# Kernel tuning notes

Hardware: AMD Instinct MI355X
Metric: run time of the kernel (lower is better)

Reference implementation:

```python
import jax, jax.numpy as jnp
import numpy as np


def setup_inputs() -> dict:
    key = jax.random.key(0)
    k1, k2 = jax.random.split(key)
    B, S, H, D = 4, 4096, 2048, 3
    hidden_states = jax.random.normal(k1, (B, S, H), dtype=jnp.float32)
    theta = jax.random.normal(k2, (D, H), dtype=jnp.float32)  # routing_params stacked [D,H]
    return {"hidden_states": hidden_states, "theta": theta}


def reference(hidden_states, theta):
    B, S, H = hidden_states.shape
    D = theta.shape[0]
    k = max(1, int(S * (1.0 / D)))  # tokens kept per depth step

    # Per-depth gemv scoring + sigmoid, all depths at once: [B,S,D]
    scores = jax.nn.sigmoid(jnp.einsum('bsh,dh->bsd', hidden_states, theta))

    depth = jnp.zeros((B, S), dtype=jnp.int32)
    active = jnp.ones((B, S), dtype=bool)
    bidx = jnp.arange(B)[:, None]  # [B,1] for batched scatter
    neg_inf = jnp.float32(-jnp.inf)

    for r in range(D):  # D is small and fixed (3)
        masked = jnp.where(active, scores[:, :, r], neg_inf)
        _, idx = jax.lax.top_k(masked, k)  # [B,k]
        depth = depth.at[bidx, idx].set(r + 1)
        step_mask = jnp.zeros((B, S), dtype=bool).at[bidx, idx].set(True)
        active = active & step_mask

    depth = jnp.where(depth == 0, 1, depth)

    # Balancing loss: note the original applies sigmoid twice (scores_list is
    # post-sigmoid, then compute_balancing_loss sigmoids again). batchmean over D.
    probs = jax.nn.sigmoid(scores).mean(axis=(0, 1))  # [D]
    target = jnp.float32(1.0 / D)
    balancing_loss = jnp.sum(target * (jnp.log(target) - jnp.log(probs))) / D

    # masks list: [ones, final_active, final_active] stacked as [D,B,S]
    masks = jnp.stack([jnp.ones((B, S), dtype=bool) if r == 0 else active
                       for r in range(D)])
    return depth, balancing_loss, masks
```

## Files before the change

### kernel.cpp

```cpp
#include <hip/hip_runtime.h>
#include <math.h>

#define BB 4
#define SS 4096
#define HH 2048
#define DD 3
#define KK 1365
#define ONEBITS 0x3f800000u
#define NW 8
#define NBLK (BB * SS / NW)

__global__ __launch_bounds__(512, 8) void score_kernel(
    const float* __restrict__ hs, const float* __restrict__ theta,
    float* __restrict__ scores0, double* __restrict__ partials,
    float* __restrict__ m0)
{
    __shared__ __align__(16) float th[DD * HH];
    __shared__ double wpart[NW][DD];

    const int tid = threadIdx.x;

    {
        const float4* src = reinterpret_cast<const float4*>(theta);
        float4* dst = reinterpret_cast<float4*>(th);
#pragma unroll
        for (int i = 0; i < 3; ++i) dst[tid + 512 * i] = src[tid + 512 * i];
    }

    const long gid = (long)blockIdx.x * 512 + tid;
    if (gid < (long)BB * SS) m0[gid] = 1.0f;

    __syncthreads();

    const int wave = tid >> 6;
    const int lane = tid & 63;
    const long token = (long)blockIdx.x * NW + wave;

    const float4* row = reinterpret_cast<const float4*>(hs + token * HH);
    const float4* t0p = reinterpret_cast<const float4*>(th);
    const float4* t1p = reinterpret_cast<const float4*>(th + HH);
    const float4* t2p = reinterpret_cast<const float4*>(th + 2 * HH);

    double a0 = 0.0, a1 = 0.0, a2 = 0.0;
#pragma unroll
    for (int j = 0; j < HH / 256; ++j) {
        const int v = j * 64 + lane;
        const float4 h  = row[v];
        const float4 x0 = t0p[v];
        const float4 x1 = t1p[v];
        const float4 x2 = t2p[v];
        a0 += (double)h.x * x0.x + (double)h.y * x0.y + (double)h.z * x0.z + (double)h.w * x0.w;
        a1 += (double)h.x * x1.x + (double)h.y * x1.y + (double)h.z * x1.z + (double)h.w * x1.w;
        a2 += (double)h.x * x2.x + (double)h.y * x2.y + (double)h.z * x2.z + (double)h.w * x2.w;
    }
#pragma unroll
    for (int off = 32; off; off >>= 1) {
        a0 += __shfl_down(a0, off);
        a1 += __shfl_down(a1, off);
        a2 += __shfl_down(a2, off);
    }

    if (lane == 0) {
        const float x0 = (float)a0, x1 = (float)a1, x2 = (float)a2;
        const float s0 = 1.0f / (1.0f + expf(-x0));
        const float s1 = 1.0f / (1.0f + expf(-x1));
        const float s2 = 1.0f / (1.0f + expf(-x2));
        scores0[token] = s0;
        wpart[wave][0] = (double)(1.0f / (1.0f + expf(-s0)));
        wpart[wave][1] = (double)(1.0f / (1.0f + expf(-s1)));
        wpart[wave][2] = (double)(1.0f / (1.0f + expf(-s2)));
    }
    __syncthreads();
    if (tid < DD) {
        const int d = tid;
        double s = 0.0;
#pragma unroll
        for (int w = 0; w < NW; ++w) s += wpart[w][d];
        partials[(long)blockIdx.x * DD + d] = s;
    }
}

__global__ __launch_bounds__(1024) void select_kernel(
    const float* __restrict__ scores0, const double* __restrict__ partials,
    float* __restrict__ out)
{
    const int tid  = threadIdx.x;
    const int lane = tid & 63;
    const int wid  = tid >> 6;
    const int blk  = blockIdx.x;

    if (blk == 12) {
        double a0 = 0.0, a1 = 0.0, a2 = 0.0;
        for (int i = tid; i < NBLK; i += 1024) {
            a0 += partials[(long)i * DD + 0];
            a1 += partials[(long)i * DD + 1];
            a2 += partials[(long)i * DD + 2];
        }
#pragma unroll
        for (int off = 32; off; off >>= 1) {
            a0 += __shfl_down(a0, off);
            a1 += __shfl_down(a1, off);
            a2 += __shfl_down(a2, off);
        }
        __shared__ double shl[DD][16];
        if (lane == 0) { shl[0][wid] = a0; shl[1][wid] = a1; shl[2][wid] = a2; }
        __syncthreads();
        if (tid == 0) {
            double p0 = 0, p1 = 0, p2 = 0;
            for (int w = 0; w < 16; ++w) { p0 += shl[0][w]; p1 += shl[1][w]; p2 += shl[2][w]; }
            const double n = (double)BB * SS;
            p0 /= n; p1 /= n; p2 /= n;
            const double t = 1.0 / 3.0;
            out[(long)BB * SS] = (float)((t * (log(t) - log(p0)) +
                                          t * (log(t) - log(p1)) +
                                          t * (log(t) - log(p2))) / 3.0);
        }
        return;
    }

    const int b = blk / 3, plane = blk % 3;
    const float* rowp = scores0 + (long)b * SS;

    __shared__ unsigned wsum[16];
    __shared__ __align__(16) unsigned su[SS];
    __shared__ unsigned whist[16 * 256];
    __shared__ unsigned wtot[4];
    __shared__ unsigned sbin, skk;

    uint4 uu = reinterpret_cast<const uint4*>(rowp)[tid];

    unsigned vstar = ONEBITS;
    unsigned e0 = (uu.x == vstar), e1 = (uu.y == vstar),
             e2 = (uu.z == vstar), e3 = (uu.w == vstar);
    unsigned cnt = e0 + e1 + e2 + e3;

    unsigned inc = cnt;
#pragma unroll
    for (int off = 1; off < 64; off <<= 1) {
        unsigned t = __shfl_up(inc, off);
        if (lane >= off) inc += t;
    }
    if (lane == 63) wsum[wid] = inc;
    __syncthreads();
    if (wid == 0) {
        unsigned wv = (lane < 16) ? wsum[lane] : 0;
#pragma unroll
        for (int off = 1; off < 16; off <<= 1) {
            unsigned t = __shfl_up(wv, off);
            if (lane >= off) wv += t;
        }
        if (lane < 16) wsum[lane] = wv;
    }
    __syncthreads();
    unsigned p     = inc - cnt + (wid > 0 ? wsum[wid - 1] : 0);
    unsigned total = wsum[15];
    unsigned rem   = KK;

    if (total < KK) {
        for (int i = tid; i < SS; i += 1024) su[i] = __float_as_uint(rowp[i]);
        unsigned prefix = 0, maskbits = 0, kk = KK;
        for (int pass = 0; pass < 4; ++pass) {
            const int shift = 24 - 8 * pass;
            for (int i = tid; i < 16 * 256; i += 1024) whist[i] = 0;
            __syncthreads();
            for (int i = tid; i < SS; i += 1024) {
                unsigned u = su[i];
                if ((u & maskbits) == prefix)
                    atomicAdd(&whist[(wid << 8) + ((u >> shift) & 255u)], 1u);
            }
            __syncthreads();
            unsigned val = 0, s = 0;
            if (tid < 256) {
                for (int w = 0; w < 16; ++w) val += whist[(w << 8) + tid];
                s = val;
#pragma unroll
                for (int off = 1; off < 64; off <<= 1) {
                    unsigned t = __shfl_down(s, off);
                    if (lane + off < 64) s += t;
                }
                if (lane == 0) wtot[wid] = s;
            }
            __syncthreads();
            if (tid < 256) {
                unsigned cge = s;
                for (int w = wid + 1; w < 4; ++w) cge += wtot[w];
                unsigned cgt = cge - val;
                if (cgt < kk && cge >= kk) { sbin = (unsigned)tid; skk = kk - cgt; }
            }
            __syncthreads();
            prefix   |= (sbin << shift);
            maskbits |= (255u << shift);
            kk = skk;
        }
        vstar = prefix;
        rem   = kk;
        e0 = (uu.x == vstar); e1 = (uu.y == vstar);
        e2 = (uu.z == vstar); e3 = (uu.w == vstar);
        cnt = e0 + e1 + e2 + e3;
        inc = cnt;
#pragma unroll
        for (int off = 1; off < 64; off <<= 1) {
            unsigned t = __shfl_up(inc, off);
            if (lane >= off) inc += t;
        }
        __syncthreads();
        if (lane == 63) wsum[wid] = inc;
        __syncthreads();
        if (wid == 0) {
            unsigned wv = (lane < 16) ? wsum[lane] : 0;
#pragma unroll
            for (int off = 1; off < 16; off <<= 1) {
                unsigned t = __shfl_up(wv, off);
                if (lane >= off) wv += t;
            }
            if (lane < 16) wsum[lane] = wv;
        }
        __syncthreads();
        p = inc - cnt + (wid > 0 ? wsum[wid - 1] : 0);
    }

    const bool sel0 = (uu.x > vstar) || (e0 && p < rem); p += e0;
    const bool sel1 = (uu.y > vstar) || (e1 && p < rem); p += e1;
    const bool sel2 = (uu.z > vstar) || (e2 && p < rem); p += e2;
    const bool sel3 = (uu.w > vstar) || (e3 && p < rem);

    if (plane == 0) {
        float4 dv = make_float4(sel0 ? 3.0f : 1.0f, sel1 ? 3.0f : 1.0f,
                                sel2 ? 3.0f : 1.0f, sel3 ? 3.0f : 1.0f);
        reinterpret_cast<float4*>(out + (long)b * SS)[tid] = dv;
    } else {
        float* m = out + (long)BB * SS + 1 + (long)plane * BB * SS + (long)b * SS;
        const int base = tid * 4;
        m[base + 0] = sel0 ? 1.0f : 0.0f;
        m[base + 1] = sel1 ? 1.0f : 0.0f;
        m[base + 2] = sel2 ? 1.0f : 0.0f;
        m[base + 3] = sel3 ? 1.0f : 0.0f;
    }
}

extern "C" void kernel_launch(void* const* d_in, const int* in_sizes, int n_in,
                              void* d_out, int out_size, void* d_ws, size_t ws_size,
                              hipStream_t stream) {
    const float* hs    = (const float*)d_in[0];
    const float* theta = (const float*)d_in[1];
    float* out = (float*)d_out;

    float*  scores0  = (float*)d_ws;
    double* partials = (double*)((char*)d_ws + (size_t)BB * SS * 4);
    float*  m0       = out + (long)BB * SS + 1;

    score_kernel <<<dim3(NBLK), dim3(512),  0, stream>>>(hs, theta, scores0, partials, m0);
    select_kernel<<<dim3(13),   dim3(1024), 0, stream>>>(scores0, partials, out);
}
```

Baseline: 37.19 us.

## Drop shared theta staging, read theta via cache and prefetch hidden row

The scoring kernel no longer copies the 24 KB theta matrix into shared memory in every block. Each wave now reads theta directly from global memory, where it should stay cache-resident, and issues all eight hidden-state float4 loads up front so they are in flight together. Blocks shrink to 256 threads (4 tokens each) with a different launch bound, and the per-block partial sum is unrolled. This removes the LDS fill and barrier before compute, at the cost of more cached global traffic for theta and more registers per thread.

```diff
diff --git a/kernel.cpp b/kernel.cpp
--- a/kernel.cpp
+++ b/kernel.cpp
@@ -7,51 +7,41 @@
 #define DD 3
 #define KK 1365
 #define ONEBITS 0x3f800000u
-#define NW 8
-#define NBLK (BB * SS / NW)
-
-__global__ __launch_bounds__(512, 8) void score_kernel(
+#define NBLK 4096
+
+__global__ __launch_bounds__(256, 6) void score_kernel(
     const float* __restrict__ hs, const float* __restrict__ theta,
     float* __restrict__ scores0, double* __restrict__ partials,
     float* __restrict__ m0)
 {
-    __shared__ __align__(16) float th[DD * HH];
-    __shared__ double wpart[NW][DD];
-
-    const int tid = threadIdx.x;
-
-    {
-        const float4* src = reinterpret_cast<const float4*>(theta);
-        float4* dst = reinterpret_cast<float4*>(th);
-#pragma unroll
-        for (int i = 0; i < 3; ++i) dst[tid + 512 * i] = src[tid + 512 * i];
-    }
-
-    const long gid = (long)blockIdx.x * 512 + tid;
-    if (gid < (long)BB * SS) m0[gid] = 1.0f;
-
-    __syncthreads();
-
+    const int tid  = threadIdx.x;
     const int wave = tid >> 6;
     const int lane = tid & 63;
-    const long token = (long)blockIdx.x * NW + wave;
+    const long token = (long)blockIdx.x * 4 + wave;
 
     const float4* row = reinterpret_cast<const float4*>(hs + token * HH);
-    const float4* t0p = reinterpret_cast<const float4*>(th);
-    const float4* t1p = reinterpret_cast<const float4*>(th + HH);
-    const float4* t2p = reinterpret_cast<const float4*>(th + 2 * HH);
+
+    float4 h[8];
+#pragma unroll
+    for (int j = 0; j < 8; ++j) h[j] = row[j * 64 + lane];
+
+    const long gid = (long)blockIdx.x * 256 + tid;
+    if (gid < (long)BB * SS) m0[gid] = 1.0f;
+
+    const float4* t0p = reinterpret_cast<const float4*>(theta);
+    const float4* t1p = reinterpret_cast<const float4*>(theta + HH);
+    const float4* t2p = reinterpret_cast<const float4*>(theta + 2 * HH);
 
     double a0 = 0.0, a1 = 0.0, a2 = 0.0;
 #pragma unroll
-    for (int j = 0; j < HH / 256; ++j) {
+    for (int j = 0; j < 8; ++j) {
         const int v = j * 64 + lane;
-        const float4 h  = row[v];
         const float4 x0 = t0p[v];
         const float4 x1 = t1p[v];
         const float4 x2 = t2p[v];
-        a0 += (double)h.x * x0.x + (double)h.y * x0.y + (double)h.z * x0.z + (double)h.w * x0.w;
-        a1 += (double)h.x * x1.x + (double)h.y * x1.y + (double)h.z * x1.z + (double)h.w * x1.w;
-        a2 += (double)h.x * x2.x + (double)h.y * x2.y + (double)h.z * x2.z + (double)h.w * x2.w;
+        a0 += (double)h[j].x * x0.x + (double)h[j].y * x0.y + (double)h[j].z * x0.z + (double)h[j].w * x0.w;
+        a1 += (double)h[j].x * x1.x + (double)h[j].y * x1.y + (double)h[j].z * x1.z + (double)h[j].w * x1.w;
+        a2 += (double)h[j].x * x2.x + (double)h[j].y * x2.y + (double)h[j].z * x2.z + (double)h[j].w * x2.w;
     }
 #pragma unroll
     for (int off = 32; off; off >>= 1) {
@@ -60,6 +50,7 @@
         a2 += __shfl_down(a2, off);
     }
 
+    __shared__ double wpart[4][DD];
     if (lane == 0) {
         const float x0 = (float)a0, x1 = (float)a1, x2 = (float)a2;
         const float s0 = 1.0f / (1.0f + expf(-x0));
@@ -71,13 +62,9 @@
         wpart[wave][2] = (double)(1.0f / (1.0f + expf(-s2)));
     }
     __syncthreads();
-    if (tid < DD) {
-        const int d = tid;
-        double s = 0.0;
-#pragma unroll
-        for (int w = 0; w < NW; ++w) s += wpart[w][d];
-        partials[(long)blockIdx.x * DD + d] = s;
-    }
+    if (tid < DD)
+        partials[(long)blockIdx.x * DD + tid] =
+            wpart[0][tid] + wpart[1][tid] + wpart[2][tid] + wpart[3][tid];
 }
 
 __global__ __launch_bounds__(1024) void select_kernel(
@@ -249,6 +236,6 @@
     double* partials = (double*)((char*)d_ws + (size_t)BB * SS * 4);
     float*  m0       = out + (long)BB * SS + 1;
 
-    score_kernel <<<dim3(NBLK), dim3(512),  0, stream>>>(hs, theta, scores0, partials, m0);
+    score_kernel <<<dim3(NBLK), dim3(256),  0, stream>>>(hs, theta, scores0, partials, m0);
     select_kernel<<<dim3(13),   dim3(1024), 0, stream>>>(scores0, partials, out);
 }
```

Result: faster. 35.60 us (-4.3%).
